# Kernel optimization log

Measured on AMD Instinct MI355X. Metric: run time of the kernel, lower is better.

The kernel has to match this reference:

```python
import jax, jax.numpy as jnp
import numpy as np

FACTOR = 2  # self.factor; anchor='edge', interpolation='linear', bound='dft', extrapolate=False


def _resize_axis_linear_dft(x, axis, osz):
    """Linear resize of one axis with periodic ('dft') boundary, anchor='edge'.

    Out-of-FOV samples (|coord| beyond [-0.5, isz-0.5]) are zeroed
    (extrapolate=False). With edge anchor this mask is always all-True,
    but we keep it for faithfulness.
    """
    isz = x.shape[axis]
    # edge anchor: output voxel centers map to input coords
    c = (jnp.arange(osz, dtype=x.dtype) + 0.5) * (isz / osz) - 0.5
    i0 = jnp.floor(c).astype(jnp.int32)
    w1 = c - i0.astype(x.dtype)          # fractional part
    i0w = jnp.mod(i0, isz)               # dft = circular wrap
    i1w = jnp.mod(i0 + 1, isz)
    x0 = jnp.take(x, i0w, axis=axis)
    x1 = jnp.take(x, i1w, axis=axis)
    # broadcast weights along `axis`
    bshape = [1] * x.ndim
    bshape[axis] = osz
    w1b = w1.reshape(bshape)
    inb = ((c >= -0.5) & (c <= isz - 0.5)).astype(x.dtype).reshape(bshape)
    return (x0 * (1.0 - w1b) + x1 * w1b) * inb


def _resize_flow(flow):
    # flow: (batch, ndim, *inshape)
    ishape = flow.shape[2:]
    oshape = tuple(int(s * FACTOR) for s in ishape)
    out = flow
    for d, osz in enumerate(oshape):
        out = _resize_axis_linear_dft(out, axis=2 + d, osz=osz)
    # anchor 'e': rescale displacement magnitude per channel by osz/isz
    scales = jnp.array([o / i for o, i in zip(oshape, ishape)], dtype=flow.dtype)
    scales = scales.reshape((1, len(ishape)) + (1,) * len(ishape))
    return out * scales


def setup_inputs() -> dict:
    key = jax.random.key(0)
    flow = jax.random.normal(key, (2, 3, 96, 96, 96), dtype=jnp.float32)
    return {"flow": flow}


def reference(flow):
    return _resize_flow(flow)
```

## Files before the change

kernel.cpp:

```cpp
#include <hip/hip_runtime.h>


#define ISZ  96
#define OSZ  192
#define NX4  48
#define NTY  48
#define NTZ2 24
#define ZSTR (ISZ * ISZ)

typedef float vf4 __attribute__((ext_vector_type(4)));

struct Q4 { float a, b, c, d; };
struct PL { Q4 r0, r1, r2, r3; };

__device__ __forceinline__ Q4 q_wsum(float wl, const Q4& L, float wh, const Q4& H) {
    Q4 q;
    q.a = fmaf(wl, L.a, wh * H.a);
    q.b = fmaf(wl, L.b, wh * H.b);
    q.c = fmaf(wl, L.c, wh * H.c);
    q.d = fmaf(wl, L.d, wh * H.d);
    return q;
}

__global__ __launch_bounds__(64)
void resize_flow_kernel(const float* __restrict__ in, float* __restrict__ out) {
    unsigned bid = blockIdx.x;
    unsigned wid = (bid & 7u) * (gridDim.x >> 3) + (bid >> 3);
    unsigned t   = wid * 64u + threadIdx.x;

    int x4 = (int)(t % NX4);
    unsigned r = t / NX4;
    int ty  = (int)(r % NTY); r /= NTY;
    int tz2 = (int)(r % NTZ2);
    int bc  = (int)(r / NTZ2);

    int xm = 2 * x4;
    int xa = (x4 == 0)       ? ISZ - 1 : xm - 1;
    int xd = (x4 == NX4 - 1) ? 0       : xm + 2;

    int jy  = 2 * ty;
    int ry0 = (jy == 0) ? ISZ - 1 : jy - 1;
    int ry1 = jy, ry2 = jy + 1;
    int ry3 = (jy + 2 == ISZ) ? 0 : jy + 2;

    int K  = 4 * tz2;
    int pm = (K == 0)        ? ISZ - 1 : K - 1;
    int pp = (K + 4 == ISZ)  ? 0       : K + 4;

    const float* base = in + (size_t)bc * (ISZ * ZSTR);

    auto ld = [&](const float* row) -> Q4 {
        float2 m = *reinterpret_cast<const float2*>(row + xm);
        Q4 q; q.a = row[xa]; q.b = m.x; q.c = m.y; q.d = row[xd];
        return q;
    };
    auto load_plane = [&](int p) -> PL {
        const float* pp_ = base + (size_t)p * ZSTR;
        PL L;
        L.r0 = ld(pp_ + ry0 * ISZ);
        L.r1 = ld(pp_ + ry1 * ISZ);
        L.r2 = ld(pp_ + ry2 * ISZ);
        L.r3 = ld(pp_ + ry3 * ISZ);
        return L;
    };
    auto yblend = [&](const PL& L, Q4* Y) {
        Y[0] = q_wsum(0.25f, L.r0, 0.75f, L.r1);
        Y[1] = q_wsum(0.75f, L.r1, 0.25f, L.r2);
        Y[2] = q_wsum(0.25f, L.r1, 0.75f, L.r2);
        Y[3] = q_wsum(0.75f, L.r2, 0.25f, L.r3);
    };

    int oyb = 4 * ty;
    auto store4 = [&](float wl, const Q4* YL, float wh, const Q4* YH, int oz) {
        float* pz = out + (((size_t)bc * OSZ + oz) * OSZ + oyb) * OSZ + 4 * x4;
#pragma unroll
        for (int i = 0; i < 4; ++i) {
            Q4 q = q_wsum(wl, YL[i], wh, YH[i]);
            vf4 o;
            o.x = fmaf(0.25f, q.a, 0.75f * q.b);
            o.y = fmaf(0.75f, q.b, 0.25f * q.c);
            o.z = fmaf(0.25f, q.b, 0.75f * q.c);
            o.w = fmaf(0.75f, q.c, 0.25f * q.d);
            *reinterpret_cast<vf4*>(pz + (size_t)i * OSZ) = o;
        }
    };

    Q4 Ya[4], Yb[4], Yc[4];
    int ozb = 8 * tz2;

    PL La = load_plane(pm);
    PL Lb = load_plane(K);
    PL Lc = load_plane(K + 1);

    yblend(La, Ya);
    yblend(Lb, Yb);
    La = load_plane(K + 2);
    store4(0.5f, Ya, 1.5f, Yb, ozb + 0);

    yblend(Lc, Yc);
    store4(1.5f, Yb, 0.5f, Yc, ozb + 1);
    store4(0.5f, Yb, 1.5f, Yc, ozb + 2);
    Lb = load_plane(K + 3);

    yblend(La, Ya);
    store4(1.5f, Yc, 0.5f, Ya, ozb + 3);
    store4(0.5f, Yc, 1.5f, Ya, ozb + 4);
    Lc = load_plane(pp);

    yblend(Lb, Yb);
    store4(1.5f, Ya, 0.5f, Yb, ozb + 5);
    store4(0.5f, Ya, 1.5f, Yb, ozb + 6);

    yblend(Lc, Yc);
    store4(1.5f, Yb, 0.5f, Yc, ozb + 7);
}

extern "C" void kernel_launch(void* const* d_in, const int* in_sizes, int n_in,
                              void* d_out, int out_size, void* d_ws, size_t ws_size,
                              hipStream_t stream) {
    const float* in = (const float*)d_in[0];
    float* out = (float*)d_out;

    int total = 6 * NTZ2 * NTY * NX4;
    int block = 64;
    int grid  = total / block;

    resize_flow_kernel<<<grid, block, 0, stream>>>(in, out);
}
```

Measured before the change: 36.09 us.

## Remap work so each block handles one input z-plane and a y-chunk

Work is redistributed so each 64-thread block handles one input z-plane and a chunk of 8 y-tiles. Each of 48 active lanes owns one x-quad and loops over y, blending the neighbouring planes k-1, k and k+1 into two output z-slices. The aim is to give each block a contiguous output region and simpler indexing, with a row-by-row y loop. In exchange, 16 of 64 lanes in every wavefront sit idle, and each thread re-reads three planes to produce two output z-slices, where the old code read six planes for eight. That raises load traffic and cache pressure on a kernel that is bound by store bandwidth.

```diff
diff --git a/kernel.cpp b/kernel.cpp
--- a/kernel.cpp
+++ b/kernel.cpp
@@ -4,14 +4,13 @@
 #define ISZ  96
 #define OSZ  192
 #define NX4  48
-#define NTY  48
-#define NTZ2 24
+#define YBC  8
+#define NYC  6
 #define ZSTR (ISZ * ISZ)
 
 typedef float vf4 __attribute__((ext_vector_type(4)));
 
 struct Q4 { float a, b, c, d; };
-struct PL { Q4 r0, r1, r2, r3; };
 
 __device__ __forceinline__ Q4 q_wsum(float wl, const Q4& L, float wh, const Q4& H) {
     Q4 q;
@@ -26,53 +25,49 @@
 void resize_flow_kernel(const float* __restrict__ in, float* __restrict__ out) {
     unsigned bid = blockIdx.x;
     unsigned wid = (bid & 7u) * (gridDim.x >> 3) + (bid >> 3);
-    unsigned t   = wid * 64u + threadIdx.x;
 
-    int x4 = (int)(t % NX4);
-    unsigned r = t / NX4;
-    int ty  = (int)(r % NTY); r /= NTY;
-    int tz2 = (int)(r % NTZ2);
-    int bc  = (int)(r / NTZ2);
+    int yc = (int)(wid % NYC);
+    unsigned r = wid / NYC;
+    int k  = (int)(r % ISZ);
+    int bc = (int)(r / ISZ);
+
+    int lane = (int)threadIdx.x;
+    if (lane >= NX4) return;
+    int x4 = lane;
 
     int xm = 2 * x4;
     int xa = (x4 == 0)       ? ISZ - 1 : xm - 1;
     int xd = (x4 == NX4 - 1) ? 0       : xm + 2;
 
-    int jy  = 2 * ty;
-    int ry0 = (jy == 0) ? ISZ - 1 : jy - 1;
-    int ry1 = jy, ry2 = jy + 1;
-    int ry3 = (jy + 2 == ISZ) ? 0 : jy + 2;
-
-    int K  = 4 * tz2;
-    int pm = (K == 0)        ? ISZ - 1 : K - 1;
-    int pp = (K + 4 == ISZ)  ? 0       : K + 4;
+    int km = (k == 0)       ? ISZ - 1 : k - 1;
+    int kp = (k == ISZ - 1) ? 0       : k + 1;
 
     const float* base = in + (size_t)bc * (ISZ * ZSTR);
+    const float* Pm = base + (size_t)km * ZSTR;
+    const float* P0 = base + (size_t)k  * ZSTR;
+    const float* Pp = base + (size_t)kp * ZSTR;
 
     auto ld = [&](const float* row) -> Q4 {
         float2 m = *reinterpret_cast<const float2*>(row + xm);
         Q4 q; q.a = row[xa]; q.b = m.x; q.c = m.y; q.d = row[xd];
         return q;
     };
-    auto load_plane = [&](int p) -> PL {
-        const float* pp_ = base + (size_t)p * ZSTR;
-        PL L;
-        L.r0 = ld(pp_ + ry0 * ISZ);
-        L.r1 = ld(pp_ + ry1 * ISZ);
-        L.r2 = ld(pp_ + ry2 * ISZ);
-        L.r3 = ld(pp_ + ry3 * ISZ);
-        return L;
-    };
-    auto yblend = [&](const PL& L, Q4* Y) {
-        Y[0] = q_wsum(0.25f, L.r0, 0.75f, L.r1);
-        Y[1] = q_wsum(0.75f, L.r1, 0.25f, L.r2);
-        Y[2] = q_wsum(0.25f, L.r1, 0.75f, L.r2);
-        Y[3] = q_wsum(0.75f, L.r2, 0.25f, L.r3);
+    auto yblend = [&](const float* P, int ry0, int ry1, int ry2, int ry3, Q4* Y) {
+        Q4 R0 = ld(P + ry0 * ISZ);
+        Q4 R1 = ld(P + ry1 * ISZ);
+        Q4 R2 = ld(P + ry2 * ISZ);
+        Q4 R3 = ld(P + ry3 * ISZ);
+        Y[0] = q_wsum(0.25f, R0, 0.75f, R1);
+        Y[1] = q_wsum(0.75f, R1, 0.25f, R2);
+        Y[2] = q_wsum(0.25f, R1, 0.75f, R2);
+        Y[3] = q_wsum(0.75f, R2, 0.25f, R3);
     };
 
-    int oyb = 4 * ty;
-    auto store4 = [&](float wl, const Q4* YL, float wh, const Q4* YH, int oz) {
-        float* pz = out + (((size_t)bc * OSZ + oz) * OSZ + oyb) * OSZ + 4 * x4;
+    float* out0 = out + (((size_t)bc * OSZ + 2 * k)     * OSZ) * OSZ + 4 * x4;
+    float* out1 = out + (((size_t)bc * OSZ + 2 * k + 1) * OSZ) * OSZ + 4 * x4;
+
+    auto store4 = [&](float wl, const Q4* YL, float wh, const Q4* YH,
+                      float* pz, int oy) {
 #pragma unroll
         for (int i = 0; i < 4; ++i) {
             Q4 q = q_wsum(wl, YL[i], wh, YH[i]);
@@ -81,38 +76,25 @@
             o.y = fmaf(0.75f, q.b, 0.25f * q.c);
             o.z = fmaf(0.25f, q.b, 0.75f * q.c);
             o.w = fmaf(0.75f, q.c, 0.25f * q.d);
-            *reinterpret_cast<vf4*>(pz + (size_t)i * OSZ) = o;
+            *reinterpret_cast<vf4*>(pz + (size_t)(oy + i) * OSZ) = o;
         }
     };
 
-    Q4 Ya[4], Yb[4], Yc[4];
-    int ozb = 8 * tz2;
+    Q4 Ym[4], Y0[4], Yp[4];
+    for (int tyl = 0; tyl < YBC; ++tyl) {
+        int ty = yc * YBC + tyl;
+        int jy = 2 * ty;
+        int ry0 = (jy == 0) ? ISZ - 1 : jy - 1;
+        int ry1 = jy, ry2 = jy + 1;
+        int ry3 = (jy + 2 == ISZ) ? 0 : jy + 2;
 
-    PL La = load_plane(pm);
-    PL Lb = load_plane(K);
-    PL Lc = load_plane(K + 1);
+        yblend(Pm, ry0, ry1, ry2, ry3, Ym);
+        yblend(P0, ry0, ry1, ry2, ry3, Y0);
+        yblend(Pp, ry0, ry1, ry2, ry3, Yp);
 
-    yblend(La, Ya);
-    yblend(Lb, Yb);
-    La = load_plane(K + 2);
-    store4(0.5f, Ya, 1.5f, Yb, ozb + 0);
-
-    yblend(Lc, Yc);
-    store4(1.5f, Yb, 0.5f, Yc, ozb + 1);
-    store4(0.5f, Yb, 1.5f, Yc, ozb + 2);
-    Lb = load_plane(K + 3);
-
-    yblend(La, Ya);
-    store4(1.5f, Yc, 0.5f, Ya, ozb + 3);
-    store4(0.5f, Yc, 1.5f, Ya, ozb + 4);
-    Lc = load_plane(pp);
-
-    yblend(Lb, Yb);
-    store4(1.5f, Ya, 0.5f, Yb, ozb + 5);
-    store4(0.5f, Ya, 1.5f, Yb, ozb + 6);
-
-    yblend(Lc, Yc);
-    store4(1.5f, Yb, 0.5f, Yc, ozb + 7);
+        store4(0.5f, Ym, 1.5f, Y0, out0, 4 * ty);
+        store4(1.5f, Y0, 0.5f, Yp, out1, 4 * ty);
+    }
 }
 
 extern "C" void kernel_launch(void* const* d_in, const int* in_sizes, int n_in,
@@ -121,9 +103,8 @@
     const float* in = (const float*)d_in[0];
     float* out = (float*)d_out;
 
-    int total = 6 * NTZ2 * NTY * NX4;
+    int grid  = 6 * ISZ * NYC;
     int block = 64;
-    int grid  = total / block;
 
     resize_flow_kernel<<<grid, block, 0, stream>>>(in, out);
 }
```

New measurement: 41.56 us. 15.1% more time.
